# Kernel optimization log

Measured on AMD Instinct MI355X. Metric: run time of the kernel, lower is better.

## Reference

```python
import jax, jax.numpy as jnp
import numpy as np

N_GRAPHS = 128   # number of graphs in the batch
G = 128          # nodes per graph (equal-sized ragged blocks for the reference)
D = 512          # node embedding dim (feature_dim)
EPS = 1e-7


def setup_inputs() -> dict:
    key = jax.random.key(0)
    embeddings = jax.random.normal(key, (N_GRAPHS * G, D), dtype=jnp.float32)
    # Precompute block-diagonal strict-upper-triangular mask as gather indices.
    # Equivalent to torch.block_diag(*[triu(ones(g,g), diagonal=1) for g in sizes]).bool()
    iu_r, iu_c = np.triu_indices(G, k=1)                 # per-block triu(.,1) indices
    offsets = (np.arange(N_GRAPHS) * G)[:, None]         # block offsets into [N, N]
    row_idx = jnp.asarray((offsets + iu_r[None, :]).ravel(), dtype=jnp.int32)
    col_idx = jnp.asarray((offsets + iu_c[None, :]).ravel(), dtype=jnp.int32)
    return {"embeddings": embeddings, "row_idx": row_idx, "col_idx": col_idx}


def reference(embeddings, row_idx, col_idx):
    # Full NxN dot-product similarity (N = total nodes across all graphs).
    sims = embeddings @ embeddings.T                     # [N, N]
    m = sims.min()
    M = sims.max()
    sims = (sims - m) / (M - m + EPS)                    # global min-max normalization
    # Gather block-diagonal strict-upper-triangular entries -> flat vector.
    return sims[row_idx, col_idx]                        # [sum_g g*(g-1)/2]
```

## Files before the change

kernel.cpp:

```cpp
#include <hip/hip_runtime.h>
#include <hip/hip_bf16.h>
#include <stdint.h>
#include <math.h>


typedef __attribute__((ext_vector_type(8))) __bf16 bf16x8;
typedef __attribute__((ext_vector_type(16))) float floatx16;
typedef __attribute__((ext_vector_type(4))) int intx4;
typedef __attribute__((ext_vector_type(16))) int intx16;

#define AS1 __attribute__((address_space(1)))
#define AS3 __attribute__((address_space(3)))

static constexpr int DIM      = 512;
static constexpr int NTILE    = 128;
static constexpr int NPART    = NTILE * (NTILE + 1) / 2;
static constexpr int CAP      = 512;
static constexpr float QS     = 19.5f;
static constexpr int MARGIN_I = 3042;


static __device__ __forceinline__ unsigned short f2bf_rne(float f) {
  unsigned int u = __float_as_uint(f);
  u += 0x7fffu + ((u >> 16) & 1u);
  return (unsigned short)(u >> 16);
}
static __device__ __forceinline__ int fkey(float f) {
  int s = __float_as_int(f);
  return s >= 0 ? s : (s ^ 0x7fffffff);
}
static __device__ __forceinline__ float funkey(int k) {
  return __int_as_float(k >= 0 ? k : (k ^ 0x7fffffff));
}
static __device__ __forceinline__ int swzi(int row, int c8) {
  return c8 ^ (row & 7) ^ ((row >> 3) & 7);
}
static __device__ __forceinline__ int swzd(int row, int c16) {
  return c16 ^ (row & 15);
}
static __device__ __forceinline__ void tri_decode(int bi, int& tr_, int& tc_) {
  int t = (int)((257.0 - sqrt(66049.0 - 8.0 * (double)bi)) * 0.5);
  if (t < 0) t = 0;
  if (t > 127) t = 127;
  while (t * (257 - t) / 2 > bi) --t;
  while (t < 127 && (t + 1) * (256 - t) / 2 <= bi) ++t;
  tr_ = t;
  tc_ = t + (bi - t * (257 - t) / 2);
}

__global__ void k_convert(const float* __restrict__ in,
                          unsigned short* __restrict__ bf,
                          char* __restrict__ q,
                          int* __restrict__ ctrl, int n4) {
  int i = blockIdx.x * blockDim.x + threadIdx.x;
  if (i == 0) {
    ctrl[0] = 0x7fffffff; ctrl[1] = (int)0x80000000;
    ctrl[2] = 0x7fffffff; ctrl[3] = (int)0x80000000;
    ctrl[4] = 0;
  }
  if (i >= n4) return;
  float4 v = ((const float4*)in)[i];
  ushort4 o;
  o.x = f2bf_rne(v.x); o.y = f2bf_rne(v.y);
  o.z = f2bf_rne(v.z); o.w = f2bf_rne(v.w);
  ((ushort4*)bf)[i] = o;
  int qx = __float2int_rn(v.x * QS), qy = __float2int_rn(v.y * QS);
  int qz = __float2int_rn(v.z * QS), qw = __float2int_rn(v.w * QS);
  char4 c;
  c.x = (char)min(127, max(-127, qx));
  c.y = (char)min(127, max(-127, qy));
  c.z = (char)min(127, max(-127, qz));
  c.w = (char)min(127, max(-127, qw));
  ((char4*)q)[i] = c;
}

__global__ __launch_bounds__(256) void k_gemm(
    const char* __restrict__ Eq,
    const unsigned short* __restrict__ E,
    int2* __restrict__ ipartials,
    float* __restrict__ diagblocks,
    int* __restrict__ ctrl) {
  int tr, tc;
  tri_decode(blockIdx.x, tr, tc);

  const int tid = threadIdx.x;
  __shared__ __align__(16) char smem[2][128 * 128];
  __shared__ float2 redbuf[4];
  __shared__ int2 iredbuf[4];

  const int w = tid >> 6, lane = tid & 63;
  const int wr = w >> 1, wc = w & 1;
  const int l31 = lane & 31;
  const int kg  = lane >> 5;

  if (tr != tc) {
    char* lA8 = smem[0];
    char* lB8 = smem[1];
    intx16 acc[2][2];
#pragma unroll
    for (int i = 0; i < 2; i++)
#pragma unroll
      for (int j = 0; j < 2; j++)
#pragma unroll
        for (int r = 0; r < 16; r++) acc[i][j][r] = 0;

    const int rowBaseA = tr * 128;
    const int rowBaseB = tc * 128;

    for (int kb = 0; kb < 4; kb++) {
      const int kBase = kb * 128;
#pragma unroll
      for (int j = 0; j < 4; j++) {
        int cb  = (w * 4 + j) * 64;
        int p   = cb + lane;
        int row = p >> 3, c8 = p & 7;
        int sc8 = swzi(row, c8);
        const char* gA = Eq + (size_t)(rowBaseA + row) * DIM + kBase + sc8 * 16;
        const char* gB = Eq + (size_t)(rowBaseB + row) * DIM + kBase + sc8 * 16;
        __builtin_amdgcn_global_load_lds((const AS1 unsigned int*)gA,
                                         (AS3 unsigned int*)(lA8 + p * 16), 16, 0, 0);
        __builtin_amdgcn_global_load_lds((const AS1 unsigned int*)gB,
                                         (AS3 unsigned int*)(lB8 + p * 16), 16, 0, 0);
      }
      __syncthreads();

#pragma unroll
      for (int ks = 0; ks < 4; ks++) {
        intx4 af[2], bfv[2];
        const int c8 = ks * 2 + kg;
#pragma unroll
        for (int t = 0; t < 2; t++) {
          int ra = wr * 64 + t * 32 + l31;
          int rb = wc * 64 + t * 32 + l31;
          af[t]  = *(const intx4*)(lA8 + ra * 128 + swzi(ra, c8) * 16);
          bfv[t] = *(const intx4*)(lB8 + rb * 128 + swzi(rb, c8) * 16);
        }
#pragma unroll
        for (int ti = 0; ti < 2; ti++)
#pragma unroll
          for (int tj = 0; tj < 2; tj++)
            acc[ti][tj] = __builtin_amdgcn_mfma_i32_32x32x32_i8(
                af[ti], bfv[tj], acc[ti][tj], 0, 0, 0);
      }
      __syncthreads();
    }

    int vmin = 0x7fffffff;
#pragma unroll
    for (int ti = 0; ti < 2; ti++)
#pragma unroll
      for (int tj = 0; tj < 2; tj++)
#pragma unroll
        for (int r = 0; r < 16; r++) vmin = min(vmin, acc[ti][tj][r]);
#pragma unroll
    for (int m_ = 32; m_ >= 1; m_ >>= 1)
      vmin = min(vmin, __shfl_xor(vmin, m_));
    if (lane == 0) iredbuf[w] = make_int2(vmin, 0);
    __syncthreads();
    if (tid == 0) {
      int mn = iredbuf[0].x;
      for (int i = 1; i < 4; i++) mn = min(mn, iredbuf[i].x);
      ipartials[blockIdx.x] = make_int2(mn, 0);
      atomicMin(&ctrl[2], mn);
    }
  } else {
    unsigned short* lA = (unsigned short*)smem[0];
    floatx16 acc[2][2];
#pragma unroll
    for (int i = 0; i < 2; i++)
#pragma unroll
      for (int j = 0; j < 2; j++)
#pragma unroll
        for (int r = 0; r < 16; r++) acc[i][j][r] = 0.f;

    const int rowBase = tr * 128;

    for (int kb = 0; kb < 4; kb++) {
      const int kBase = kb * 128;
#pragma unroll
      for (int j = 0; j < 8; j++) {
        int cb  = (w * 8 + j) * 64;
        int p   = cb + lane;
        int row = p >> 4, c16 = p & 15;
        int sc = swzd(row, c16);
        const unsigned short* gA =
            E + (size_t)(rowBase + row) * DIM + kBase + sc * 8;
        __builtin_amdgcn_global_load_lds((const AS1 unsigned int*)gA,
                                         (AS3 unsigned int*)(lA + p * 8), 16, 0, 0);
      }
      __syncthreads();

#pragma unroll
      for (int ks = 0; ks < 8; ks++) {
        bf16x8 af[2], bfv[2];
        const int c16 = ks * 2 + kg;
#pragma unroll
        for (int t = 0; t < 2; t++) {
          int ra = wr * 64 + t * 32 + l31;
          int rb = wc * 64 + t * 32 + l31;
          af[t]  = *(const bf16x8*)(lA + ra * 128 + swzd(ra, c16) * 8);
          bfv[t] = *(const bf16x8*)(lA + rb * 128 + swzd(rb, c16) * 8);
        }
#pragma unroll
        for (int ti = 0; ti < 2; ti++)
#pragma unroll
          for (int tj = 0; tj < 2; tj++)
            acc[ti][tj] = __builtin_amdgcn_mfma_f32_32x32x16_bf16(
                af[ti], bfv[tj], acc[ti][tj], 0, 0, 0);
      }
      __syncthreads();
    }

    float vmin = 3.4e38f, vmax = -3.4e38f;
#pragma unroll
    for (int ti = 0; ti < 2; ti++)
#pragma unroll
      for (int tj = 0; tj < 2; tj++)
#pragma unroll
        for (int r = 0; r < 16; r++) {
          float v = acc[ti][tj][r];
          vmin = fminf(vmin, v);
          vmax = fmaxf(vmax, v);
        }
#pragma unroll
    for (int m_ = 32; m_ >= 1; m_ >>= 1) {
      vmin = fminf(vmin, __shfl_xor(vmin, m_));
      vmax = fmaxf(vmax, __shfl_xor(vmax, m_));
    }
    if (lane == 0) redbuf[w] = make_float2(vmin, vmax);
    __syncthreads();
    if (tid == 0) {
      float mn = redbuf[0].x, mx = redbuf[0].y;
      for (int i = 1; i < 4; i++) {
        mn = fminf(mn, redbuf[i].x);
        mx = fmaxf(mx, redbuf[i].y);
      }
      atomicMin(&ctrl[0], fkey(mn));
      atomicMax(&ctrl[1], fkey(mx));
      ipartials[blockIdx.x] = make_int2(0x7fffffff, 0);
    }

    float* Bout = diagblocks + (size_t)tr * (128 * 128);
#pragma unroll
    for (int ti = 0; ti < 2; ti++) {
#pragma unroll
      for (int tj = 0; tj < 2; tj++) {
        int cbase = wc * 64 + tj * 32 + l31;
#pragma unroll
        for (int r = 0; r < 16; r++) {
          int row = wr * 64 + ti * 32 + (r & 3) + 8 * (r >> 2) + 4 * kg;
          Bout[row * 128 + cbase] = acc[ti][tj][r];
        }
      }
    }
  }
}

__global__ void k_flag(const int2* __restrict__ ipartials,
                       int* __restrict__ ctrl, int* __restrict__ list) {
  int i = blockIdx.x * blockDim.x + threadIdx.x;
  if (i >= NPART) return;
  int gmin = ctrl[2];
  if (ipartials[i].x <= gmin + MARGIN_I) {
    int pos = atomicAdd(&ctrl[4], 1);
    if (pos < CAP) {
      int tr, tc;
      tri_decode(i, tr, tc);
      list[pos] = (tr << 8) | tc;
    }
  }
}

__global__ __launch_bounds__(256) void k_refine(
    const unsigned short* __restrict__ E,
    const int* __restrict__ list, int* __restrict__ ctrl) {
  int cnt = ctrl[4];
  if (cnt > CAP) cnt = CAP;
  if ((int)blockIdx.x >= cnt) return;
  const int enc = list[blockIdx.x];
  const int tr = enc >> 8, tc = enc & 255;

  const int tid = threadIdx.x;
  __shared__ __align__(16) unsigned short lA[128 * 64];
  __shared__ __align__(16) unsigned short lB[128 * 64];
  __shared__ float2 redbuf[4];

  const int w = tid >> 6, lane = tid & 63;
  const int wr = w >> 1, wc = w & 1;
  const int l31 = lane & 31;
  const int kg  = lane >> 5;

  floatx16 acc[2][2];
#pragma unroll
  for (int i = 0; i < 2; i++)
#pragma unroll
    for (int j = 0; j < 2; j++)
#pragma unroll
      for (int r = 0; r < 16; r++) acc[i][j][r] = 0.f;

  const int rowBaseA = tr * 128;
  const int rowBaseB = tc * 128;

  for (int kb = 0; kb < 8; kb++) {
    const int kBase = kb * 64;
#pragma unroll
    for (int j = 0; j < 4; j++) {
      int cb  = (w * 4 + j) * 64;
      int p   = cb + lane;
      int row = p >> 3, c8 = p & 7;
      int sc8 = c8 ^ (row & 7);
      const unsigned short* gA = E + (size_t)(rowBaseA + row) * DIM + kBase + sc8 * 8;
      const unsigned short* gB = E + (size_t)(rowBaseB + row) * DIM + kBase + sc8 * 8;
      __builtin_amdgcn_global_load_lds((const AS1 unsigned int*)gA,
                                       (AS3 unsigned int*)(lA + cb * 8), 16, 0, 0);
      __builtin_amdgcn_global_load_lds((const AS1 unsigned int*)gB,
                                       (AS3 unsigned int*)(lB + cb * 8), 16, 0, 0);
    }
    __syncthreads();

#pragma unroll
    for (int ks = 0; ks < 4; ks++) {
      bf16x8 af[2], bfv[2];
      const int c8 = ks * 2 + kg;
#pragma unroll
      for (int t = 0; t < 2; t++) {
        int ra = wr * 64 + t * 32 + l31;
        int rb = wc * 64 + t * 32 + l31;
        af[t]  = *(const bf16x8*)(lA + (ra * 8 + (c8 ^ (ra & 7))) * 8);
        bfv[t] = *(const bf16x8*)(lB + (rb * 8 + (c8 ^ (rb & 7))) * 8);
      }
#pragma unroll
      for (int ti = 0; ti < 2; ti++)
#pragma unroll
        for (int tj = 0; tj < 2; tj++)
          acc[ti][tj] = __builtin_amdgcn_mfma_f32_32x32x16_bf16(
              af[ti], bfv[tj], acc[ti][tj], 0, 0, 0);
    }
    __syncthreads();
  }

  float vmin = 3.4e38f;
#pragma unroll
  for (int ti = 0; ti < 2; ti++)
#pragma unroll
    for (int tj = 0; tj < 2; tj++)
#pragma unroll
      for (int r = 0; r < 16; r++) vmin = fminf(vmin, acc[ti][tj][r]);
#pragma unroll
  for (int m_ = 32; m_ >= 1; m_ >>= 1)
    vmin = fminf(vmin, __shfl_xor(vmin, m_));
  if (lane == 0) redbuf[w] = make_float2(vmin, 0.f);
  __syncthreads();
  if (tid == 0) {
    float mn = redbuf[0].x;
    for (int i = 1; i < 4; i++) mn = fminf(mn, redbuf[i].x);
    atomicMin(&ctrl[0], fkey(mn));
  }
}

__global__ __launch_bounds__(256) void k_gather(
    const int* __restrict__ rix, const int* __restrict__ cix,
    const float* __restrict__ blocks, const int* __restrict__ ctrl,
    float* __restrict__ out, int n) {
  int i = blockIdx.x * blockDim.x + threadIdx.x;
  if (i >= n) return;
  float m   = funkey(ctrl[0]);
  float M   = funkey(ctrl[1]);
  float inv = 1.0f / (M - m + 1e-7f);
  int r = rix[i], c = cix[i];
  int g = r >> 7;
  float v = blocks[((size_t)g << 14) + ((r & 127) << 7) + (c & 127)];
  out[i] = (v - m) * inv;
}

extern "C" void kernel_launch(void* const* d_in, const int* in_sizes, int n_in,
                              void* d_out, int out_size, void* d_ws, size_t ws_size,
                              hipStream_t stream) {
  const float* emb = (const float*)d_in[0];
  const int* rix   = (const int*)d_in[1];
  const int* cix   = (const int*)d_in[2];

  char* ws = (char*)d_ws;
  int* ctrl           = (int*)ws;
  unsigned short* Ebf = (unsigned short*)(ws + 256);
  char* Eq            = (char*)(ws + 256 + (16u << 20));
  float* diagblocks   = (float*)(ws + 256 + (24u << 20));
  int2* ipartials     = (int2*)(ws + 256 + (32u << 20));
  int* list           = (int*)(ws + 256 + (32u << 20) + (128u << 10));

  int n_elem = in_sizes[0];
  int n4 = n_elem / 4;
  k_convert<<<(n4 + 255) / 256, 256, 0, stream>>>(emb, Ebf, Eq, ctrl, n4);

  k_gemm<<<NPART, 256, 0, stream>>>(Eq, Ebf, ipartials, diagblocks, ctrl);

  k_flag<<<(NPART + 255) / 256, 256, 0, stream>>>(ipartials, ctrl, list);

  k_refine<<<CAP, 256, 0, stream>>>(Ebf, list, ctrl);

  k_gather<<<(out_size + 255) / 256, 256, 0, stream>>>(rix, cix, diagblocks,
                                                       ctrl, (float*)d_out,
                                                       out_size);
}
```

Measured before the change: 208.5 us.

## Fuse all stages into one persistent cooperative kernel with grid syncs

Replaces the five-kernel pipeline (convert, gemm, flag, refine, gather) with a single cooperative persistent kernel. Stages are separated by grid.sync and blocks loop over tiles in grid-stride fashion. The flag and list compaction is replaced by an inline check of each tile's partial min against the global min plus a margin. This removes launch gaps between kernels, at the cost of grid-wide barriers, a grid capped at 1024 blocks, and uneven refine work across blocks.

```diff
diff --git a/kernel.cpp b/kernel.cpp
--- a/kernel.cpp
+++ b/kernel.cpp
@@ -1,8 +1,11 @@
 #include <hip/hip_runtime.h>
+#include <hip/hip_cooperative_groups.h>
 #include <hip/hip_bf16.h>
 #include <stdint.h>
 #include <math.h>
 
+
+namespace cg = cooperative_groups;
 
 typedef __attribute__((ext_vector_type(8))) __bf16 bf16x8;
 typedef __attribute__((ext_vector_type(16))) float floatx16;
@@ -37,6 +40,9 @@
 }
 static __device__ __forceinline__ int swzd(int row, int c16) {
   return c16 ^ (row & 15);
+}
+static __device__ __forceinline__ int swz8(int row, int c8) {
+  return c8 ^ (row & 7);
 }
 static __device__ __forceinline__ void tri_decode(int bi, int& tr_, int& tc_) {
   int t = (int)((257.0 - sqrt(66049.0 - 8.0 * (double)bi)) * 0.5);
@@ -46,6 +52,316 @@
   while (t < 127 && (t + 1) * (256 - t) / 2 <= bi) ++t;
   tr_ = t;
   tc_ = t + (bi - t * (257 - t) / 2);
+}
+
+__global__ __launch_bounds__(256) void k_mega(
+    const float* __restrict__ in,
+    unsigned short* __restrict__ Ebf,
+    char* __restrict__ Eq,
+    int2* __restrict__ ipart,
+    float* __restrict__ diagblocks,
+    int* __restrict__ ctrl,
+    const int* __restrict__ rix,
+    const int* __restrict__ cix,
+    float* __restrict__ out,
+    int out_size, int n4) {
+  cg::grid_group grid = cg::this_grid();
+
+  __shared__ __align__(16) char smem[2][16384];
+  __shared__ float2 redbuf[4];
+  __shared__ int2 iredbuf[4];
+
+  const int tid = threadIdx.x;
+  const int w = tid >> 6, lane = tid & 63;
+  const int wr = w >> 1, wc = w & 1;
+  const int l31 = lane & 31;
+  const int kg  = lane >> 5;
+  const int gstride = gridDim.x * blockDim.x;
+
+  if (blockIdx.x == 0 && tid == 0) {
+    ctrl[0] = 0x7fffffff; ctrl[1] = (int)0x80000000;
+    ctrl[2] = 0x7fffffff; ctrl[3] = (int)0x80000000;
+    ctrl[4] = 0;
+  }
+  for (int i = blockIdx.x * blockDim.x + tid; i < n4; i += gstride) {
+    float4 v = ((const float4*)in)[i];
+    ushort4 o;
+    o.x = f2bf_rne(v.x); o.y = f2bf_rne(v.y);
+    o.z = f2bf_rne(v.z); o.w = f2bf_rne(v.w);
+    ((ushort4*)Ebf)[i] = o;
+    int qx = __float2int_rn(v.x * QS), qy = __float2int_rn(v.y * QS);
+    int qz = __float2int_rn(v.z * QS), qw = __float2int_rn(v.w * QS);
+    char4 c;
+    c.x = (char)min(127, max(-127, qx));
+    c.y = (char)min(127, max(-127, qy));
+    c.z = (char)min(127, max(-127, qz));
+    c.w = (char)min(127, max(-127, qw));
+    ((char4*)Eq)[i] = c;
+  }
+  __threadfence();
+  grid.sync();
+
+  for (int bi = blockIdx.x; bi < NPART; bi += gridDim.x) {
+    int tr, tc;
+    tri_decode(bi, tr, tc);
+
+    if (tr != tc) {
+      char* lA8 = smem[0];
+      char* lB8 = smem[1];
+      intx16 acc[2][2];
+#pragma unroll
+      for (int i = 0; i < 2; i++)
+#pragma unroll
+        for (int j = 0; j < 2; j++)
+#pragma unroll
+          for (int r = 0; r < 16; r++) acc[i][j][r] = 0;
+
+      const int rowBaseA = tr * 128;
+      const int rowBaseB = tc * 128;
+
+      for (int kb = 0; kb < 4; kb++) {
+        const int kBase = kb * 128;
+#pragma unroll
+        for (int j = 0; j < 4; j++) {
+          int cb  = (w * 4 + j) * 64;
+          int p   = cb + lane;
+          int row = p >> 3, c8 = p & 7;
+          int sc8 = swzi(row, c8);
+          const char* gA = Eq + (size_t)(rowBaseA + row) * DIM + kBase + sc8 * 16;
+          const char* gB = Eq + (size_t)(rowBaseB + row) * DIM + kBase + sc8 * 16;
+          __builtin_amdgcn_global_load_lds((const AS1 unsigned int*)gA,
+                                           (AS3 unsigned int*)(lA8 + p * 16), 16, 0, 0);
+          __builtin_amdgcn_global_load_lds((const AS1 unsigned int*)gB,
+                                           (AS3 unsigned int*)(lB8 + p * 16), 16, 0, 0);
+        }
+        __syncthreads();
+
+#pragma unroll
+        for (int ks = 0; ks < 4; ks++) {
+          intx4 af[2], bfv[2];
+          const int c8 = ks * 2 + kg;
+#pragma unroll
+          for (int t = 0; t < 2; t++) {
+            int ra = wr * 64 + t * 32 + l31;
+            int rb = wc * 64 + t * 32 + l31;
+            af[t]  = *(const intx4*)(lA8 + ra * 128 + swzi(ra, c8) * 16);
+            bfv[t] = *(const intx4*)(lB8 + rb * 128 + swzi(rb, c8) * 16);
+          }
+#pragma unroll
+          for (int ti = 0; ti < 2; ti++)
+#pragma unroll
+            for (int tj = 0; tj < 2; tj++)
+              acc[ti][tj] = __builtin_amdgcn_mfma_i32_32x32x32_i8(
+                  af[ti], bfv[tj], acc[ti][tj], 0, 0, 0);
+        }
+        __syncthreads();
+      }
+
+      int vmin = 0x7fffffff;
+#pragma unroll
+      for (int ti = 0; ti < 2; ti++)
+#pragma unroll
+        for (int tj = 0; tj < 2; tj++)
+#pragma unroll
+          for (int r = 0; r < 16; r++) vmin = min(vmin, acc[ti][tj][r]);
+#pragma unroll
+      for (int m_ = 32; m_ >= 1; m_ >>= 1)
+        vmin = min(vmin, __shfl_xor(vmin, m_));
+      if (lane == 0) iredbuf[w] = make_int2(vmin, 0);
+      __syncthreads();
+      if (tid == 0) {
+        int mn = iredbuf[0].x;
+        for (int i = 1; i < 4; i++) mn = min(mn, iredbuf[i].x);
+        ipart[bi] = make_int2(mn, 0);
+        atomicMin(&ctrl[2], mn);
+      }
+    } else {
+      unsigned short* lA = (unsigned short*)&smem[0][0];
+      floatx16 acc[2][2];
+#pragma unroll
+      for (int i = 0; i < 2; i++)
+#pragma unroll
+        for (int j = 0; j < 2; j++)
+#pragma unroll
+          for (int r = 0; r < 16; r++) acc[i][j][r] = 0.f;
+
+      const int rowBase = tr * 128;
+
+      for (int kb = 0; kb < 4; kb++) {
+        const int kBase = kb * 128;
+#pragma unroll
+        for (int j = 0; j < 8; j++) {
+          int cb  = (w * 8 + j) * 64;
+          int p   = cb + lane;
+          int row = p >> 4, c16 = p & 15;
+          int sc = swzd(row, c16);
+          const unsigned short* gA =
+              Ebf + (size_t)(rowBase + row) * DIM + kBase + sc * 8;
+          __builtin_amdgcn_global_load_lds((const AS1 unsigned int*)gA,
+                                           (AS3 unsigned int*)(lA + p * 8), 16, 0, 0);
+        }
+        __syncthreads();
+
+#pragma unroll
+        for (int ks = 0; ks < 8; ks++) {
+          bf16x8 af[2], bfv[2];
+          const int c16 = ks * 2 + kg;
+#pragma unroll
+          for (int t = 0; t < 2; t++) {
+            int ra = wr * 64 + t * 32 + l31;
+            int rb = wc * 64 + t * 32 + l31;
+            af[t]  = *(const bf16x8*)(lA + ra * 128 + swzd(ra, c16) * 8);
+            bfv[t] = *(const bf16x8*)(lA + rb * 128 + swzd(rb, c16) * 8);
+          }
+#pragma unroll
+          for (int ti = 0; ti < 2; ti++)
+#pragma unroll
+            for (int tj = 0; tj < 2; tj++)
+              acc[ti][tj] = __builtin_amdgcn_mfma_f32_32x32x16_bf16(
+                  af[ti], bfv[tj], acc[ti][tj], 0, 0, 0);
+        }
+        __syncthreads();
+      }
+
+      float vmin = 3.4e38f, vmax = -3.4e38f;
+#pragma unroll
+      for (int ti = 0; ti < 2; ti++)
+#pragma unroll
+        for (int tj = 0; tj < 2; tj++)
+#pragma unroll
+          for (int r = 0; r < 16; r++) {
+            float v = acc[ti][tj][r];
+            vmin = fminf(vmin, v);
+            vmax = fmaxf(vmax, v);
+          }
+#pragma unroll
+      for (int m_ = 32; m_ >= 1; m_ >>= 1) {
+        vmin = fminf(vmin, __shfl_xor(vmin, m_));
+        vmax = fmaxf(vmax, __shfl_xor(vmax, m_));
+      }
+      if (lane == 0) redbuf[w] = make_float2(vmin, vmax);
+      __syncthreads();
+      if (tid == 0) {
+        float mn = redbuf[0].x, mx = redbuf[0].y;
+        for (int i = 1; i < 4; i++) {
+          mn = fminf(mn, redbuf[i].x);
+          mx = fmaxf(mx, redbuf[i].y);
+        }
+        atomicMin(&ctrl[0], fkey(mn));
+        atomicMax(&ctrl[1], fkey(mx));
+        ipart[bi] = make_int2(0x7fffffff, 0);
+      }
+
+      float* Bout = diagblocks + (size_t)tr * (128 * 128);
+#pragma unroll
+      for (int ti = 0; ti < 2; ti++) {
+#pragma unroll
+        for (int tj = 0; tj < 2; tj++) {
+          int cbase = wc * 64 + tj * 32 + l31;
+#pragma unroll
+          for (int r = 0; r < 16; r++) {
+            int row = wr * 64 + ti * 32 + (r & 3) + 8 * (r >> 2) + 4 * kg;
+            Bout[row * 128 + cbase] = acc[ti][tj][r];
+          }
+        }
+      }
+    }
+    __syncthreads();
+  }
+  __threadfence();
+  grid.sync();
+
+  {
+    const int gmin = ctrl[2];
+    for (int bi = blockIdx.x; bi < NPART; bi += gridDim.x) {
+      if (ipart[bi].x > gmin + MARGIN_I) continue;
+      int tr, tc;
+      tri_decode(bi, tr, tc);
+      unsigned short* lA = (unsigned short*)&smem[0][0];
+      unsigned short* lB = (unsigned short*)&smem[1][0];
+      floatx16 acc[2][2];
+#pragma unroll
+      for (int i = 0; i < 2; i++)
+#pragma unroll
+        for (int j = 0; j < 2; j++)
+#pragma unroll
+          for (int r = 0; r < 16; r++) acc[i][j][r] = 0.f;
+
+      const int rowBaseA = tr * 128;
+      const int rowBaseB = tc * 128;
+
+      for (int kb = 0; kb < 8; kb++) {
+        const int kBase = kb * 64;
+#pragma unroll
+        for (int j = 0; j < 4; j++) {
+          int cb  = (w * 4 + j) * 64;
+          int p   = cb + lane;
+          int row = p >> 3, c8 = p & 7;
+          int sc8 = swz8(row, c8);
+          const unsigned short* gA = Ebf + (size_t)(rowBaseA + row) * DIM + kBase + sc8 * 8;
+          const unsigned short* gB = Ebf + (size_t)(rowBaseB + row) * DIM + kBase + sc8 * 8;
+          __builtin_amdgcn_global_load_lds((const AS1 unsigned int*)gA,
+                                           (AS3 unsigned int*)(lA + cb * 8), 16, 0, 0);
+          __builtin_amdgcn_global_load_lds((const AS1 unsigned int*)gB,
+                                           (AS3 unsigned int*)(lB + cb * 8), 16, 0, 0);
+        }
+        __syncthreads();
+
+#pragma unroll
+        for (int ks = 0; ks < 4; ks++) {
+          bf16x8 af[2], bfv[2];
+          const int c8 = ks * 2 + kg;
+#pragma unroll
+          for (int t = 0; t < 2; t++) {
+            int ra = wr * 64 + t * 32 + l31;
+            int rb = wc * 64 + t * 32 + l31;
+            af[t]  = *(const bf16x8*)(lA + (ra * 8 + swz8(ra, c8)) * 8);
+            bfv[t] = *(const bf16x8*)(lB + (rb * 8 + swz8(rb, c8)) * 8);
+          }
+#pragma unroll
+          for (int ti = 0; ti < 2; ti++)
+#pragma unroll
+            for (int tj = 0; tj < 2; tj++)
+              acc[ti][tj] = __builtin_amdgcn_mfma_f32_32x32x16_bf16(
+                  af[ti], bfv[tj], acc[ti][tj], 0, 0, 0);
+        }
+        __syncthreads();
+      }
+
+      float vmin = 3.4e38f;
+#pragma unroll
+      for (int ti = 0; ti < 2; ti++)
+#pragma unroll
+        for (int tj = 0; tj < 2; tj++)
+#pragma unroll
+          for (int r = 0; r < 16; r++) vmin = fminf(vmin, acc[ti][tj][r]);
+#pragma unroll
+      for (int m_ = 32; m_ >= 1; m_ >>= 1)
+        vmin = fminf(vmin, __shfl_xor(vmin, m_));
+      if (lane == 0) redbuf[w] = make_float2(vmin, 0.f);
+      __syncthreads();
+      if (tid == 0) {
+        float mn = redbuf[0].x;
+        for (int i = 1; i < 4; i++) mn = fminf(mn, redbuf[i].x);
+        atomicMin(&ctrl[0], fkey(mn));
+      }
+      __syncthreads();
+    }
+  }
+  __threadfence();
+  grid.sync();
+
+  {
+    const float m   = funkey(ctrl[0]);
+    const float M   = funkey(ctrl[1]);
+    const float inv = 1.0f / (M - m + 1e-7f);
+    for (int i = blockIdx.x * blockDim.x + tid; i < out_size; i += gstride) {
+      int r = rix[i], c = cix[i];
+      int g = r >> 7;
+      float v = diagblocks[((size_t)g << 14) + ((r & 127) << 7) + (c & 127)];
+      out[i] = (v - m) * inv;
+    }
+  }
 }
 
 __global__ void k_convert(const float* __restrict__ in,
@@ -84,7 +400,7 @@
   tri_decode(blockIdx.x, tr, tc);
 
   const int tid = threadIdx.x;
-  __shared__ __align__(16) char smem[2][128 * 128];
+  __shared__ __align__(16) char smem[2][16384];
   __shared__ float2 redbuf[4];
   __shared__ int2 iredbuf[4];
 
@@ -164,7 +480,7 @@
       atomicMin(&ctrl[2], mn);
     }
   } else {
-    unsigned short* lA = (unsigned short*)smem[0];
+    unsigned short* lA = (unsigned short*)&smem[0][0];
     floatx16 acc[2][2];
 #pragma unroll
     for (int i = 0; i < 2; i++)
@@ -308,7 +624,7 @@
       int cb  = (w * 4 + j) * 64;
       int p   = cb + lane;
       int row = p >> 3, c8 = p & 7;
-      int sc8 = c8 ^ (row & 7);
+      int sc8 = swz8(row, c8);
       const unsigned short* gA = E + (size_t)(rowBaseA + row) * DIM + kBase + sc8 * 8;
       const unsigned short* gB = E + (size_t)(rowBaseB + row) * DIM + kBase + sc8 * 8;
       __builtin_amdgcn_global_load_lds((const AS1 unsigned int*)gA,
@@ -326,8 +642,8 @@
       for (int t = 0; t < 2; t++) {
         int ra = wr * 64 + t * 32 + l31;
         int rb = wc * 64 + t * 32 + l31;
-        af[t]  = *(const bf16x8*)(lA + (ra * 8 + (c8 ^ (ra & 7))) * 8);
-        bfv[t] = *(const bf16x8*)(lB + (rb * 8 + (c8 ^ (rb & 7))) * 8);
+        af[t]  = *(const bf16x8*)(lA + (ra * 8 + swz8(ra, c8)) * 8);
+        bfv[t] = *(const bf16x8*)(lB + (rb * 8 + swz8(rb, c8)) * 8);
       }
 #pragma unroll
       for (int ti = 0; ti < 2; ti++)
@@ -379,6 +695,7 @@
   const float* emb = (const float*)d_in[0];
   const int* rix   = (const int*)d_in[1];
   const int* cix   = (const int*)d_in[2];
+  float* outp      = (float*)d_out;
 
   char* ws = (char*)d_ws;
   int* ctrl           = (int*)ws;
@@ -388,17 +705,28 @@
   int2* ipartials     = (int2*)(ws + 256 + (32u << 20));
   int* list           = (int*)(ws + 256 + (32u << 20) + (128u << 10));
 
-  int n_elem = in_sizes[0];
-  int n4 = n_elem / 4;
+  int n4 = in_sizes[0] / 4;
+
+  int nblk = 0;
+  hipError_t qerr = hipOccupancyMaxActiveBlocksPerMultiprocessor(
+      &nblk, reinterpret_cast<const void*>(k_mega), 256, 0);
+  if (qerr == hipSuccess && nblk > 0) {
+    int grid = nblk * 256;
+    if (grid > 1024) grid = 1024;
+    int osz = out_size;
+    void* args[] = {(void*)&emb, (void*)&Ebf, (void*)&Eq, (void*)&ipartials,
+                    (void*)&diagblocks, (void*)&ctrl, (void*)&rix, (void*)&cix,
+                    (void*)&outp, (void*)&osz, (void*)&n4};
+    hipError_t lerr = hipLaunchCooperativeKernel(
+        reinterpret_cast<const void*>(k_mega), dim3(grid), dim3(256), args, 0,
+        stream);
+    if (lerr == hipSuccess) return;
+  }
+
   k_convert<<<(n4 + 255) / 256, 256, 0, stream>>>(emb, Ebf, Eq, ctrl, n4);
-
   k_gemm<<<NPART, 256, 0, stream>>>(Eq, Ebf, ipartials, diagblocks, ctrl);
-
   k_flag<<<(NPART + 255) / 256, 256, 0, stream>>>(ipartials, ctrl, list);
-
   k_refine<<<CAP, 256, 0, stream>>>(Ebf, list, ctrl);
-
   k_gather<<<(out_size + 255) / 256, 256, 0, stream>>>(rix, cix, diagblocks,
-                                                       ctrl, (float*)d_out,
-                                                       out_size);
-}
+                                                       ctrl, outp, out_size);
+}
```

New measurement: 209.7 us. No clear change (+0.6%).

## Pair off-diagonal int8 tiles per block and drop flag kernel

Applied to the files above, without the earlier changes.

The int8 GEMM grid becomes 65x128. Each off-diagonal block now computes two adjacent column tiles (128x256) while sharing the A tile, which halves A loads per output and uses the triangle structure without tri_decode. The separate k_flag compaction kernel is removed. k_refine now launches one block per pair index, checks its partial min against the global min plus a margin, and refines up to two tiles. This saves one launch and the atomic list, but adds many early-exit blocks, more accumulator registers per thread and a larger LDS footprint, both of which may lower occupancy.

```diff
diff --git a/kernel.cpp b/kernel.cpp
--- a/kernel.cpp
+++ b/kernel.cpp
@@ -1,7 +1,6 @@
 #include <hip/hip_runtime.h>
 #include <hip/hip_bf16.h>
 #include <stdint.h>
-#include <math.h>
 
 
 typedef __attribute__((ext_vector_type(8))) __bf16 bf16x8;
@@ -14,8 +13,7 @@
 
 static constexpr int DIM      = 512;
 static constexpr int NTILE    = 128;
-static constexpr int NPART    = NTILE * (NTILE + 1) / 2;
-static constexpr int CAP      = 512;
+static constexpr int NPAIRIDX = 65 * 128;
 static constexpr float QS     = 19.5f;
 static constexpr int MARGIN_I = 3042;
 
@@ -38,14 +36,8 @@
 static __device__ __forceinline__ int swzd(int row, int c16) {
   return c16 ^ (row & 15);
 }
-static __device__ __forceinline__ void tri_decode(int bi, int& tr_, int& tc_) {
-  int t = (int)((257.0 - sqrt(66049.0 - 8.0 * (double)bi)) * 0.5);
-  if (t < 0) t = 0;
-  if (t > 127) t = 127;
-  while (t * (257 - t) / 2 > bi) --t;
-  while (t < 127 && (t + 1) * (256 - t) / 2 <= bi) ++t;
-  tr_ = t;
-  tc_ = t + (bi - t * (257 - t) / 2);
+static __device__ __forceinline__ int swz8(int row, int c8) {
+  return c8 ^ (row & 7);
 }
 
 __global__ void k_convert(const float* __restrict__ in,
@@ -55,8 +47,7 @@
   int i = blockIdx.x * blockDim.x + threadIdx.x;
   if (i == 0) {
     ctrl[0] = 0x7fffffff; ctrl[1] = (int)0x80000000;
-    ctrl[2] = 0x7fffffff; ctrl[3] = (int)0x80000000;
-    ctrl[4] = 0;
+    ctrl[2] = 0x7fffffff;
   }
   if (i >= n4) return;
   float4 v = ((const float4*)in)[i];
@@ -77,94 +68,117 @@
 __global__ __launch_bounds__(256) void k_gemm(
     const char* __restrict__ Eq,
     const unsigned short* __restrict__ E,
-    int2* __restrict__ ipartials,
+    int* __restrict__ ipart,
     float* __restrict__ diagblocks,
     int* __restrict__ ctrl) {
-  int tr, tc;
-  tri_decode(blockIdx.x, tr, tc);
+  const int x  = blockIdx.x;
+  const int tr = blockIdx.y;
+  const int pi = tr * 65 + x;
 
   const int tid = threadIdx.x;
-  __shared__ __align__(16) char smem[2][128 * 128];
+  __shared__ __align__(16) char smem[3][16384];
   __shared__ float2 redbuf[4];
-  __shared__ int2 iredbuf[4];
+  __shared__ int iredbuf[4];
 
   const int w = tid >> 6, lane = tid & 63;
   const int wr = w >> 1, wc = w & 1;
   const int l31 = lane & 31;
   const int kg  = lane >> 5;
 
-  if (tr != tc) {
-    char* lA8 = smem[0];
-    char* lB8 = smem[1];
-    intx16 acc[2][2];
-#pragma unroll
-    for (int i = 0; i < 2; i++)
-#pragma unroll
-      for (int j = 0; j < 2; j++)
-#pragma unroll
-        for (int r = 0; r < 16; r++) acc[i][j][r] = 0;
-
-    const int rowBaseA = tr * 128;
-    const int rowBaseB = tc * 128;
+  if (x < 64) {
+    const int tc1 = 2 * x + 1;
+    if (tc1 <= tr) {
+      if (tid == 0) ipart[pi] = 0x7fffffff;
+      return;
+    }
+    const int tc0 = (2 * x > tr) ? 2 * x : tc1;
+
+    char* lA  = smem[0];
+    char* lB0 = smem[1];
+    char* lB1 = smem[2];
+
+    intx16 acc[2][2][2];
+#pragma unroll
+    for (int b = 0; b < 2; b++)
+#pragma unroll
+      for (int i = 0; i < 2; i++)
+#pragma unroll
+        for (int j = 0; j < 2; j++)
+#pragma unroll
+          for (int r = 0; r < 16; r++) acc[b][i][j][r] = 0;
+
+    const int rowBaseA  = tr * 128;
+    const int rowBaseB0 = tc0 * 128;
+    const int rowBaseB1 = tc1 * 128;
 
     for (int kb = 0; kb < 4; kb++) {
       const int kBase = kb * 128;
 #pragma unroll
       for (int j = 0; j < 4; j++) {
-        int cb  = (w * 4 + j) * 64;
-        int p   = cb + lane;
+        int p   = (w * 4 + j) * 64 + lane;
         int row = p >> 3, c8 = p & 7;
         int sc8 = swzi(row, c8);
-        const char* gA = Eq + (size_t)(rowBaseA + row) * DIM + kBase + sc8 * 16;
-        const char* gB = Eq + (size_t)(rowBaseB + row) * DIM + kBase + sc8 * 16;
+        int off = kBase + sc8 * 16;
+        const char* gA  = Eq + (size_t)(rowBaseA  + row) * DIM + off;
+        const char* gB0 = Eq + (size_t)(rowBaseB0 + row) * DIM + off;
+        const char* gB1 = Eq + (size_t)(rowBaseB1 + row) * DIM + off;
         __builtin_amdgcn_global_load_lds((const AS1 unsigned int*)gA,
-                                         (AS3 unsigned int*)(lA8 + p * 16), 16, 0, 0);
-        __builtin_amdgcn_global_load_lds((const AS1 unsigned int*)gB,
-                                         (AS3 unsigned int*)(lB8 + p * 16), 16, 0, 0);
+                                         (AS3 unsigned int*)(lA + p * 16), 16, 0, 0);
+        __builtin_amdgcn_global_load_lds((const AS1 unsigned int*)gB0,
+                                         (AS3 unsigned int*)(lB0 + p * 16), 16, 0, 0);
+        __builtin_amdgcn_global_load_lds((const AS1 unsigned int*)gB1,
+                                         (AS3 unsigned int*)(lB1 + p * 16), 16, 0, 0);
       }
       __syncthreads();
 
 #pragma unroll
       for (int ks = 0; ks < 4; ks++) {
-        intx4 af[2], bfv[2];
+        intx4 af[2], b0v[2], b1v[2];
         const int c8 = ks * 2 + kg;
 #pragma unroll
         for (int t = 0; t < 2; t++) {
           int ra = wr * 64 + t * 32 + l31;
           int rb = wc * 64 + t * 32 + l31;
-          af[t]  = *(const intx4*)(lA8 + ra * 128 + swzi(ra, c8) * 16);
-          bfv[t] = *(const intx4*)(lB8 + rb * 128 + swzi(rb, c8) * 16);
+          af[t]  = *(const intx4*)(lA  + ra * 128 + swzi(ra, c8) * 16);
+          b0v[t] = *(const intx4*)(lB0 + rb * 128 + swzi(rb, c8) * 16);
+          b1v[t] = *(const intx4*)(lB1 + rb * 128 + swzi(rb, c8) * 16);
         }
 #pragma unroll
         for (int ti = 0; ti < 2; ti++)
 #pragma unroll
-          for (int tj = 0; tj < 2; tj++)
-            acc[ti][tj] = __builtin_amdgcn_mfma_i32_32x32x32_i8(
-                af[ti], bfv[tj], acc[ti][tj], 0, 0, 0);
+          for (int tj = 0; tj < 2; tj++) {
+            acc[0][ti][tj] = __builtin_amdgcn_mfma_i32_32x32x32_i8(
+                af[ti], b0v[tj], acc[0][ti][tj], 0, 0, 0);
+            acc[1][ti][tj] = __builtin_amdgcn_mfma_i32_32x32x32_i8(
+                af[ti], b1v[tj], acc[1][ti][tj], 0, 0, 0);
+          }
       }
       __syncthreads();
     }
 
     int vmin = 0x7fffffff;
 #pragma unroll
-    for (int ti = 0; ti < 2; ti++)
-#pragma unroll
-      for (int tj = 0; tj < 2; tj++)
-#pragma unroll
-        for (int r = 0; r < 16; r++) vmin = min(vmin, acc[ti][tj][r]);
+    for (int b = 0; b < 2; b++)
+#pragma unroll
+      for (int ti = 0; ti < 2; ti++)
+#pragma unroll
+        for (int tj = 0; tj < 2; tj++)
+#pragma unroll
+          for (int r = 0; r < 16; r++) vmin = min(vmin, acc[b][ti][tj][r]);
 #pragma unroll
     for (int m_ = 32; m_ >= 1; m_ >>= 1)
       vmin = min(vmin, __shfl_xor(vmin, m_));
-    if (lane == 0) iredbuf[w] = make_int2(vmin, 0);
+    if (lane == 0) iredbuf[w] = vmin;
     __syncthreads();
     if (tid == 0) {
-      int mn = iredbuf[0].x;
-      for (int i = 1; i < 4; i++) mn = min(mn, iredbuf[i].x);
-      ipartials[blockIdx.x] = make_int2(mn, 0);
+      int mn = iredbuf[0];
+      for (int i = 1; i < 4; i++) mn = min(mn, iredbuf[i]);
+      ipart[pi] = mn;
       atomicMin(&ctrl[2], mn);
     }
   } else {
-    unsigned short* lA = (unsigned short*)smem[0];
+    if (tid == 0) ipart[pi] = 0x7fffffff;
+    unsigned short* lA = (unsigned short*)&smem[0][0];
     floatx16 acc[2][2];
 #pragma unroll
     for (int i = 0; i < 2; i++)
@@ -179,8 +193,7 @@
       const int kBase = kb * 128;
 #pragma unroll
       for (int j = 0; j < 8; j++) {
-        int cb  = (w * 8 + j) * 64;
-        int p   = cb + lane;
+        int p   = (w * 8 + j) * 64 + lane;
         int row = p >> 4, c16 = p & 15;
         int sc = swzd(row, c16);
         const unsigned short* gA =
@@ -237,7 +250,6 @@
       }
       atomicMin(&ctrl[0], fkey(mn));
       atomicMax(&ctrl[1], fkey(mx));
-      ipartials[blockIdx.x] = make_int2(0x7fffffff, 0);
     }
 
     float* Bout = diagblocks + (size_t)tr * (128 * 128);
@@ -256,105 +268,95 @@
   }
 }
 
-__global__ void k_flag(const int2* __restrict__ ipartials,
-                       int* __restrict__ ctrl, int* __restrict__ list) {
-  int i = blockIdx.x * blockDim.x + threadIdx.x;
-  if (i >= NPART) return;
-  int gmin = ctrl[2];
-  if (ipartials[i].x <= gmin + MARGIN_I) {
-    int pos = atomicAdd(&ctrl[4], 1);
-    if (pos < CAP) {
-      int tr, tc;
-      tri_decode(i, tr, tc);
-      list[pos] = (tr << 8) | tc;
-    }
-  }
-}
-
 __global__ __launch_bounds__(256) void k_refine(
     const unsigned short* __restrict__ E,
-    const int* __restrict__ list, int* __restrict__ ctrl) {
-  int cnt = ctrl[4];
-  if (cnt > CAP) cnt = CAP;
-  if ((int)blockIdx.x >= cnt) return;
-  const int enc = list[blockIdx.x];
-  const int tr = enc >> 8, tc = enc & 255;
+    const int* __restrict__ ipart, int* __restrict__ ctrl) {
+  const int pi = blockIdx.x;
+  if (ipart[pi] > ctrl[2] + MARGIN_I) return;
+  const int tr = pi / 65, x = pi % 65;
+  if (x == 64) return;
 
   const int tid = threadIdx.x;
   __shared__ __align__(16) unsigned short lA[128 * 64];
   __shared__ __align__(16) unsigned short lB[128 * 64];
-  __shared__ float2 redbuf[4];
+  __shared__ float redbuf[4];
 
   const int w = tid >> 6, lane = tid & 63;
   const int wr = w >> 1, wc = w & 1;
   const int l31 = lane & 31;
   const int kg  = lane >> 5;
 
-  floatx16 acc[2][2];
-#pragma unroll
-  for (int i = 0; i < 2; i++)
-#pragma unroll
-    for (int j = 0; j < 2; j++)
-#pragma unroll
-      for (int r = 0; r < 16; r++) acc[i][j][r] = 0.f;
-
-  const int rowBaseA = tr * 128;
-  const int rowBaseB = tc * 128;
-
-  for (int kb = 0; kb < 8; kb++) {
-    const int kBase = kb * 64;
-#pragma unroll
-    for (int j = 0; j < 4; j++) {
-      int cb  = (w * 4 + j) * 64;
-      int p   = cb + lane;
-      int row = p >> 3, c8 = p & 7;
-      int sc8 = c8 ^ (row & 7);
-      const unsigned short* gA = E + (size_t)(rowBaseA + row) * DIM + kBase + sc8 * 8;
-      const unsigned short* gB = E + (size_t)(rowBaseB + row) * DIM + kBase + sc8 * 8;
-      __builtin_amdgcn_global_load_lds((const AS1 unsigned int*)gA,
-                                       (AS3 unsigned int*)(lA + cb * 8), 16, 0, 0);
-      __builtin_amdgcn_global_load_lds((const AS1 unsigned int*)gB,
-                                       (AS3 unsigned int*)(lB + cb * 8), 16, 0, 0);
-    }
+  for (int s = 0; s < 2; s++) {
+    const int tc = 2 * x + s;
+    if (tc <= tr) continue;
+
+    floatx16 acc[2][2];
+#pragma unroll
+    for (int i = 0; i < 2; i++)
+#pragma unroll
+      for (int j = 0; j < 2; j++)
+#pragma unroll
+        for (int r = 0; r < 16; r++) acc[i][j][r] = 0.f;
+
+    const int rowBaseA = tr * 128;
+    const int rowBaseB = tc * 128;
+
+    for (int kb = 0; kb < 8; kb++) {
+      const int kBase = kb * 64;
+#pragma unroll
+      for (int j = 0; j < 4; j++) {
+        int cb  = (w * 4 + j) * 64;
+        int p   = cb + lane;
+        int row = p >> 3, c8 = p & 7;
+        int sc8 = swz8(row, c8);
+        const unsigned short* gA = E + (size_t)(rowBaseA + row) * DIM + kBase + sc8 * 8;
+        const unsigned short* gB = E + (size_t)(rowBaseB + row) * DIM + kBase + sc8 * 8;
+        __builtin_amdgcn_global_load_lds((const AS1 unsigned int*)gA,
+                                         (AS3 unsigned int*)(lA + cb * 8), 16, 0, 0);
+        __builtin_amdgcn_global_load_lds((const AS1 unsigned int*)gB,
+                                         (AS3 unsigned int*)(lB + cb * 8), 16, 0, 0);
+      }
+      __syncthreads();
+
+#pragma unroll
+      for (int ks = 0; ks < 4; ks++) {
+        bf16x8 af[2], bfv[2];
+        const int c8 = ks * 2 + kg;
+#pragma unroll
+        for (int t = 0; t < 2; t++) {
+          int ra = wr * 64 + t * 32 + l31;
+          int rb = wc * 64 + t * 32 + l31;
+          af[t]  = *(const bf16x8*)(lA + (ra * 8 + swz8(ra, c8)) * 8);
+          bfv[t] = *(const bf16x8*)(lB + (rb * 8 + swz8(rb, c8)) * 8);
+        }
+#pragma unroll
+        for (int ti = 0; ti < 2; ti++)
+#pragma unroll
+          for (int tj = 0; tj < 2; tj++)
+            acc[ti][tj] = __builtin_amdgcn_mfma_f32_32x32x16_bf16(
+                af[ti], bfv[tj], acc[ti][tj], 0, 0, 0);
+      }
+      __syncthreads();
+    }
+
+    float vmin = 3.4e38f;
+#pragma unroll
+    for (int ti = 0; ti < 2; ti++)
+#pragma unroll
+      for (int tj = 0; tj < 2; tj++)
+#pragma unroll
+        for (int r = 0; r < 16; r++) vmin = fminf(vmin, acc[ti][tj][r]);
+#pragma unroll
+    for (int m_ = 32; m_ >= 1; m_ >>= 1)
+      vmin = fminf(vmin, __shfl_xor(vmin, m_));
+    if (lane == 0) redbuf[w] = vmin;
     __syncthreads();
-
-#pragma unroll
-    for (int ks = 0; ks < 4; ks++) {
-      bf16x8 af[2], bfv[2];
-      const int c8 = ks * 2 + kg;
-#pragma unroll
-      for (int t = 0; t < 2; t++) {
-        int ra = wr * 64 + t * 32 + l31;
-        int rb = wc * 64 + t * 32 + l31;
-        af[t]  = *(const bf16x8*)(lA + (ra * 8 + (c8 ^ (ra & 7))) * 8);
-        bfv[t] = *(const bf16x8*)(lB + (rb * 8 + (c8 ^ (rb & 7))) * 8);
-      }
-#pragma unroll
-      for (int ti = 0; ti < 2; ti++)
-#pragma unroll
-        for (int tj = 0; tj < 2; tj++)
-          acc[ti][tj] = __builtin_amdgcn_mfma_f32_32x32x16_bf16(
-              af[ti], bfv[tj], acc[ti][tj], 0, 0, 0);
+    if (tid == 0) {
+      float mn = redbuf[0];
+      for (int i = 1; i < 4; i++) mn = fminf(mn, redbuf[i]);
+      atomicMin(&ctrl[0], fkey(mn));
     }
     __syncthreads();
-  }
-
-  float vmin = 3.4e38f;
-#pragma unroll
-  for (int ti = 0; ti < 2; ti++)
-#pragma unroll
-    for (int tj = 0; tj < 2; tj++)
-#pragma unroll
-      for (int r = 0; r < 16; r++) vmin = fminf(vmin, acc[ti][tj][r]);
-#pragma unroll
-  for (int m_ = 32; m_ >= 1; m_ >>= 1)
-    vmin = fminf(vmin, __shfl_xor(vmin, m_));
-  if (lane == 0) redbuf[w] = make_float2(vmin, 0.f);
-  __syncthreads();
-  if (tid == 0) {
-    float mn = redbuf[0].x;
-    for (int i = 1; i < 4; i++) mn = fminf(mn, redbuf[i].x);
-    atomicMin(&ctrl[0], fkey(mn));
   }
 }
 
@@ -385,18 +387,15 @@
   unsigned short* Ebf = (unsigned short*)(ws + 256);
   char* Eq            = (char*)(ws + 256 + (16u << 20));
   float* diagblocks   = (float*)(ws + 256 + (24u << 20));
-  int2* ipartials     = (int2*)(ws + 256 + (32u << 20));
-  int* list           = (int*)(ws + 256 + (32u << 20) + (128u << 10));
-
-  int n_elem = in_sizes[0];
-  int n4 = n_elem / 4;
+  int* ipart          = (int*)(ws + 256 + (32u << 20));
+
+  int n4 = in_sizes[0] / 4;
+
   k_convert<<<(n4 + 255) / 256, 256, 0, stream>>>(emb, Ebf, Eq, ctrl, n4);
 
-  k_gemm<<<NPART, 256, 0, stream>>>(Eq, Ebf, ipartials, diagblocks, ctrl);
-
-  k_flag<<<(NPART + 255) / 256, 256, 0, stream>>>(ipartials, ctrl, list);
-
-  k_refine<<<CAP, 256, 0, stream>>>(Ebf, list, ctrl);
+  k_gemm<<<dim3(65, 128), 256, 0, stream>>>(Eq, Ebf, ipart, diagblocks, ctrl);
+
+  k_refine<<<NPAIRIDX, 256, 0, stream>>>(Ebf, ipart, ctrl);
 
   k_gather<<<(out_size + 255) / 256, 256, 0, stream>>>(rix, cix, diagblocks,
                                                        ctrl, (float*)d_out,
```

Measured after the change: 193.4 us. 7.2% less time.
